# Kernel optimization log

Hardware: AMD Instinct MI355X
Metric: run time of the kernel (lower is better)

The kernel has to match this reference:

```python
import jax, jax.numpy as jnp
import numpy as np
from jax import lax

D_TEMPORAL, D_INNER, D_STATE, D_CONV, DT_RANK = 2, 4, 16, 4, 1
EPS = 1e-5


def setup_inputs() -> dict:
    key = jax.random.key(0)
    ks = jax.random.split(key, 14)
    B, L = 16, 32768
    f = lambda k, s, scale=1.0: jax.random.normal(k, s, jnp.float32) * scale
    dt_b = float(np.log(np.expm1(0.01)))  # softplus^-1(0.01), typical dt init
    A_log = jnp.log(jnp.tile(jnp.arange(1, D_STATE + 1, dtype=jnp.float32), (D_INNER, 1)))
    return {
        "hidden_states": f(ks[0], (B, D_TEMPORAL, L)),
        "norm_w": jnp.ones((D_TEMPORAL,), jnp.float32),
        "in_proj_w": f(ks[1], (2 * D_INNER, D_TEMPORAL), 0.5),
        "conv_w": f(ks[2], (D_INNER, D_CONV), 0.3),
        "conv_b": f(ks[3], (D_INNER,), 0.1),
        "x_proj_w": f(ks[4], (DT_RANK + 2 * D_STATE, D_INNER), 0.3),
        "dt_proj_w": f(ks[5], (D_INNER, DT_RANK), 1.0),
        "dt_proj_b": jnp.full((D_INNER,), dt_b, jnp.float32),
        "A_log": A_log,
        "D": jnp.ones((D_INNER,), jnp.float32),
        "conv_w_b": f(ks[6], (D_INNER, D_CONV), 0.3),
        "conv_b_b": f(ks[7], (D_INNER,), 0.1),
        "x_proj_w_b": f(ks[8], (DT_RANK + 2 * D_STATE, D_INNER), 0.3),
        "dt_proj_w_b": f(ks[9], (D_INNER, DT_RANK), 1.0),
        "dt_proj_b_b": jnp.full((D_INNER,), dt_b, jnp.float32),
        "A_b_log": A_log,
        "D_b": jnp.ones((D_INNER,), jnp.float32),
        "out_proj_w": f(ks[10], (D_TEMPORAL, D_INNER), 0.3),
        "norm_f_w": jnp.ones((D_TEMPORAL,), jnp.float32),
    }


def _silu(x):
    return x * jax.nn.sigmoid(x)


def _rmsnorm(x, w):
    return x * lax.rsqrt(jnp.mean(x * x, axis=-1, keepdims=True) + EPS) * w


def _branch(x, z, conv_w, conv_b, x_proj_w, dt_proj_w, dt_proj_b, A_log, D):
    # x, z: (B, d_inner, L). Causal depthwise conv + silu.
    Bb, d, L = x.shape
    xc = lax.conv_general_dilated(
        x, conv_w[:, None, :], (1,), [(D_CONV - 1, 0)],
        feature_group_count=d, dimension_numbers=("NCH", "OIH", "NCH"))
    u = _silu(xc + conv_b[None, :, None]).transpose(0, 2, 1)      # (B, L, d)
    x_dbl = u @ x_proj_w.T                                        # (B, L, rank+2n)
    dt, Bm, Cm = jnp.split(x_dbl, [DT_RANK, DT_RANK + D_STATE], axis=-1)
    dt = jax.nn.softplus(dt @ dt_proj_w.T + dt_proj_b)            # (B, L, d)
    A = -jnp.exp(A_log)                                           # (d, n)
    dA = jnp.exp(dt[..., None] * A)                               # (B, L, d, n)
    dBu = (dt * u)[..., None] * Bm[:, :, None, :]                 # (B, L, d, n)

    def step(h, inp):
        dA_t, dBu_t, C_t = inp
        h = dA_t * h + dBu_t                                      # (B, d, n)
        return h, jnp.einsum("bdn,bn->bd", h, C_t)

    h0 = jnp.zeros((Bb, d, D_STATE), dtype=u.dtype)
    _, ys = lax.scan(step, h0, (jnp.swapaxes(dA, 0, 1), jnp.swapaxes(dBu, 0, 1), jnp.swapaxes(Cm, 0, 1)))
    y = jnp.swapaxes(ys, 0, 1) + u * D                            # (B, L, d)
    return y * _silu(z.transpose(0, 2, 1))


def _forward(hidden_states, norm_w, in_proj_w, conv_w, conv_b, x_proj_w, dt_proj_w,
             dt_proj_b, A_log, D, conv_w_b, conv_b_b, x_proj_w_b, dt_proj_w_b,
             dt_proj_b_b, A_b_log, D_b, out_proj_w, norm_f_w):
    # hidden_states: (B, T=d_temporal, L); scan runs over L.
    hs = jnp.swapaxes(hidden_states, 1, 2)                        # (B, L, T)
    residual = hs.astype(jnp.float32)
    hs = _rmsnorm(residual, norm_w)
    xz = jnp.swapaxes(hs @ in_proj_w.T, 1, 2)                     # (B, 2*d_inner, L)
    x, z = jnp.split(xz, 2, axis=1)
    y_f = _branch(x, z, conv_w, conv_b, x_proj_w, dt_proj_w, dt_proj_b, A_log, D)
    y_b = _branch(x[..., ::-1], z[..., ::-1], conv_w_b, conv_b_b, x_proj_w_b,
                  dt_proj_w_b, dt_proj_b_b, A_b_log, D_b)
    y = y_f + y_b[:, ::-1, :]                                     # (B, L, d_inner)
    out = y @ out_proj_w.T                                        # (B, L, T)
    out = _rmsnorm(out + residual, norm_f_w)
    return jnp.swapaxes(out, 1, 2)                                # (B, T, L)


def reference(hidden_states, norm_w, in_proj_w, conv_w, conv_b, x_proj_w, dt_proj_w,
              dt_proj_b, A_log, D, conv_w_b, conv_b_b, x_proj_w_b, dt_proj_w_b,
              dt_proj_b_b, A_b_log, D_b, out_proj_w, norm_f_w):
    return _forward(hidden_states, norm_w, in_proj_w, conv_w, conv_b, x_proj_w,
                    dt_proj_w, dt_proj_b, A_log, D, conv_w_b, conv_b_b, x_proj_w_b,
                    dt_proj_w_b, dt_proj_b_b, A_b_log, D_b, out_proj_w, norm_f_w)
```

## Files before the change

kernel.cpp:

```cpp
#include <hip/hip_runtime.h>
#include <hip/hip_bf16.h>
#include <cstdint>

#define BB 16
#define LL 32768
#define NC 512

#define WD_SZ 256
#define XPW 0
#define CVW 132
#define CVB 148
#define DTW 152
#define DTB 156
#define AW  160
#define DW  224
#define G_INPROJ 512
#define G_NORMW 528
#define G_OUTP 530
#define G_NORMF 538
#define FLG 1000

#define PQ_OFF 4096
#define PQ_BYTES ((size_t)BB*2*NC*64*8)
#define HIN_OFF (PQ_OFF + PQ_BYTES)

__device__ __forceinline__ float bf2f(unsigned short u){ return __uint_as_float(((unsigned int)u)<<16); }
__device__ __forceinline__ float blo(unsigned int u){ return __uint_as_float(u<<16); }
__device__ __forceinline__ float bhi(unsigned int u){ return __uint_as_float(u & 0xffff0000u); }
__device__ __forceinline__ unsigned short f2bf(float f){
  unsigned int x = __float_as_uint(f);
  x += 0x7fffu + ((x>>16)&1u);
  return (unsigned short)(x>>16);
}
__device__ __forceinline__ unsigned int pack2(float a, float b){
  __hip_bfloat162 h = __float22bfloat162_rn(make_float2(a,b));
  union { __hip_bfloat162 h2; unsigned int u; } cv; cv.h2 = h;
  return cv.u;
}
__device__ __forceinline__ float siluf(float x){
  return x * __builtin_amdgcn_rcpf(1.f + __expf(-x));
}
__device__ __forceinline__ float softplusf_(float x){
  return fmaxf(x,0.f) + 0.69314718056f*__log2f(1.f + __expf(-fabsf(x)));
}
__device__ __forceinline__ float rowsum16(float x){
  union { float f; int i; } a, t;
  a.f = x;
  t.i = __builtin_amdgcn_update_dpp(0, a.i, 0x121, 0xf, 0xf, true); a.f += t.f;
  t.i = __builtin_amdgcn_update_dpp(0, a.i, 0x122, 0xf, 0xf, true); a.f += t.f;
  t.i = __builtin_amdgcn_update_dpp(0, a.i, 0x124, 0xf, 0xf, true); a.f += t.f;
  t.i = __builtin_amdgcn_update_dpp(0, a.i, 0x128, 0xf, 0xf, true); a.f += t.f;
  return a.f;
}
__device__ __forceinline__ float ldw(const void* p, int i, int isf){
  return isf ? ((const float*)p)[i] : bf2f(((const unsigned short*)p)[i]);
}
__device__ __forceinline__ float2 hid2(const void* hid, int isf, int b, int t){
  if (isf){
    const float* p = (const float*)hid;
    return make_float2(p[(size_t)b*2*LL + t], p[(size_t)b*2*LL + LL + t]);
  }
  const unsigned short* p = (const unsigned short*)hid;
  return make_float2(bf2f(p[(size_t)b*2*LL + t]), bf2f(p[(size_t)b*2*LL + LL + t]));
}
__device__ __forceinline__ float4 xrow(const void* __restrict__ hid, int isf,
                                       const float* __restrict__ W, int b, int t){
  float2 h = hid2(hid, isf, b, t);
  float ms = rsqrtf(0.5f*(h.x*h.x + h.y*h.y) + 1e-5f);
  float v0 = h.x*ms*W[G_NORMW], v1 = h.y*ms*W[G_NORMW+1];
  float4 x;
  x.x = W[G_INPROJ+0]*v0 + W[G_INPROJ+1]*v1;
  x.y = W[G_INPROJ+2]*v0 + W[G_INPROJ+3]*v1;
  x.z = W[G_INPROJ+4]*v0 + W[G_INPROJ+5]*v1;
  x.w = W[G_INPROJ+6]*v0 + W[G_INPROJ+7]*v1;
  return x;
}

__global__ void k_prep(const void* __restrict__ normw, const void* __restrict__ inpj,
    const void* __restrict__ cwf, const void* __restrict__ cbf,
    const void* __restrict__ xpf, const void* __restrict__ dwf,
    const void* __restrict__ dbf, const void* __restrict__ alf,
    const void* __restrict__ ddf,
    const void* __restrict__ cwb, const void* __restrict__ cbb,
    const void* __restrict__ xpb, const void* __restrict__ dwb,
    const void* __restrict__ dbb, const void* __restrict__ alb,
    const void* __restrict__ ddb,
    const void* __restrict__ outp, const void* __restrict__ nfw,
    float* __restrict__ W)
{
  const int isf = (((const unsigned int*)ddf)[0] == 0x3F800000u) ? 1 : 0;
  int t = threadIdx.x;
  for (int i=t;i<132;i+=256){ W[XPW+i]=ldw(xpf,i,isf); W[WD_SZ+XPW+i]=ldw(xpb,i,isf); }
  for (int i=t;i<16;i+=256){ W[CVW+i]=ldw(cwf,i,isf); W[WD_SZ+CVW+i]=ldw(cwb,i,isf); W[G_INPROJ+i]=ldw(inpj,i,isf); }
  for (int i=t;i<4;i+=256){
    W[CVB+i]=ldw(cbf,i,isf); W[WD_SZ+CVB+i]=ldw(cbb,i,isf);
    W[DTW+i]=ldw(dwf,i,isf); W[WD_SZ+DTW+i]=ldw(dwb,i,isf);
    W[DTB+i]=ldw(dbf,i,isf); W[WD_SZ+DTB+i]=ldw(dbb,i,isf);
    W[DW+i] =ldw(ddf,i,isf); W[WD_SZ+DW+i] =ldw(ddb,i,isf);
  }
  for (int i=t;i<64;i+=256){
    W[AW+i]       = -__expf(ldw(alf,i,isf)) * 1.44269504089f;
    W[WD_SZ+AW+i] = -__expf(ldw(alb,i,isf)) * 1.44269504089f;
  }
  for (int i=t;i<8;i+=256) W[G_OUTP+i]=ldw(outp,i,isf);
  for (int i=t;i<2;i+=256){ W[G_NORMW+i]=ldw(normw,i,isf); W[G_NORMF+i]=ldw(nfw,i,isf); }
  if (t==0) W[FLG] = (float)isf;
}

__global__ __launch_bounds__(128) void k_chunk(const void* __restrict__ hid,
    const float* __restrict__ W, float2* __restrict__ PQ)
{
  __shared__ __align__(16) unsigned int   DUc[2][2][4*68];
  __shared__ __align__(16) unsigned short Bsc[2][2][16*72];
  __shared__ __align__(16) float4 xbc[2][70];
  const int lane = threadIdx.x & 63;
  const int w    = threadIdx.x >> 6;
  const int gid  = blockIdx.x*2 + w;
  const int c    = gid & (NC-1);
  const int b    = gid >> 9;
  const int isf  = (int)W[FLG];

  {
    int t = c*64 + lane;
    xbc[w][lane+3] = xrow(hid, isf, W, b, t);
    if (lane < 3){
      int t2 = c*64 - 3 + lane;
      float4 v = make_float4(0.f,0.f,0.f,0.f);
      if (t2 >= 0) v = xrow(hid, isf, W, b, t2);
      xbc[w][lane] = v;
    }
    if (lane >= 61){
      int t3 = c*64 + lane + 3;
      float4 v = make_float4(0.f,0.f,0.f,0.f);
      if (t3 < LL) v = xrow(hid, isf, W, b, t3);
      xbc[w][lane+6] = v;
    }
  }
  __syncthreads();
  {
    float4 xk0=xbc[w][lane],xk1=xbc[w][lane+1],xk2=xbc[w][lane+2],xk3=xbc[w][lane+3];
    float4 xk4=xbc[w][lane+4],xk5=xbc[w][lane+5],xk6=xbc[w][lane+6];
    float uf[4], ub[4];
    uf[0] = siluf(W[CVB+0] + W[CVW+ 0]*xk0.x + W[CVW+ 1]*xk1.x + W[CVW+ 2]*xk2.x + W[CVW+ 3]*xk3.x);
    uf[1] = siluf(W[CVB+1] + W[CVW+ 4]*xk0.y + W[CVW+ 5]*xk1.y + W[CVW+ 6]*xk2.y + W[CVW+ 7]*xk3.y);
    uf[2] = siluf(W[CVB+2] + W[CVW+ 8]*xk0.z + W[CVW+ 9]*xk1.z + W[CVW+10]*xk2.z + W[CVW+11]*xk3.z);
    uf[3] = siluf(W[CVB+3] + W[CVW+12]*xk0.w + W[CVW+13]*xk1.w + W[CVW+14]*xk2.w + W[CVW+15]*xk3.w);
    const float* Wb = W + WD_SZ;
    ub[0] = siluf(Wb[CVB+0] + Wb[CVW+ 0]*xk6.x + Wb[CVW+ 1]*xk5.x + Wb[CVW+ 2]*xk4.x + Wb[CVW+ 3]*xk3.x);
    ub[1] = siluf(Wb[CVB+1] + Wb[CVW+ 4]*xk6.y + Wb[CVW+ 5]*xk5.y + Wb[CVW+ 6]*xk4.y + Wb[CVW+ 7]*xk3.y);
    ub[2] = siluf(Wb[CVB+2] + Wb[CVW+ 8]*xk6.z + Wb[CVW+ 9]*xk5.z + Wb[CVW+10]*xk4.z + Wb[CVW+11]*xk3.z);
    ub[3] = siluf(Wb[CVB+3] + Wb[CVW+12]*xk6.w + Wb[CVW+13]*xk5.w + Wb[CVW+14]*xk4.w + Wb[CVW+15]*xk3.w);
    #pragma unroll
    for (int dr=0; dr<2; dr++){
      const float* Wd = W + dr*WD_SZ;
      const float* uu = dr ? ub : uf;
      float dtr = Wd[XPW+0]*uu[0]+Wd[XPW+1]*uu[1]+Wd[XPW+2]*uu[2]+Wd[XPW+3]*uu[3];
      #pragma unroll
      for (int d2=0; d2<4; d2++){
        float dt = softplusf_(fmaf(Wd[DTW+d2], dtr, Wd[DTB+d2]));
        DUc[w][dr][d2*68+lane] = pack2(dt, dt*uu[d2]);
      }
      #pragma unroll
      for (int n=0;n<16;n++){
        float Bn = Wd[XPW+(1+n)*4+0]*uu[0]+Wd[XPW+(1+n)*4+1]*uu[1]
                 + Wd[XPW+(1+n)*4+2]*uu[2]+Wd[XPW+(1+n)*4+3]*uu[3];
        Bsc[w][dr][n*72+lane] = f2bf(Bn);
      }
    }
  }
  __syncthreads();
  const int d = lane>>4, n = lane&15;
  const float Af = W[AW + d*16 + n];
  const float Ab = W[WD_SZ + AW + d*16 + n];
  float Pf=1.f, Qf=0.f, Pb=1.f, Qb=0.f;
  for (int j4=0; j4<16; j4++){
    const int t0f = j4*4, t0b = 60 - j4*4;
    uint4 uf4 = *(const uint4*)&DUc[w][0][d*68+t0f];
    uint4 ub4 = *(const uint4*)&DUc[w][1][d*68+t0b];
    ushort4 bf4 = *(const ushort4*)&Bsc[w][0][n*72+t0f];
    ushort4 bb4 = *(const ushort4*)&Bsc[w][1][n*72+t0b];
    unsigned int ufa[4]={uf4.x,uf4.y,uf4.z,uf4.w}, uba[4]={ub4.x,ub4.y,ub4.z,ub4.w};
    unsigned short bfa[4]={bf4.x,bf4.y,bf4.z,bf4.w}, bba[4]={bb4.x,bb4.y,bb4.z,bb4.w};
    #pragma unroll
    for (int jr=0; jr<4; jr++){
      float e = exp2f(Af*blo(ufa[jr]));
      Pf *= e;
      Qf = fmaf(Qf, e, bhi(ufa[jr])*bf2f(bfa[jr]));
      const int k = 3-jr;
      float eb = exp2f(Ab*blo(uba[k]));
      Pb *= eb;
      Qb = fmaf(Qb, eb, bhi(uba[k])*bf2f(bba[k]));
    }
  }
  PQ[((size_t)(b*2+0)*NC + c)*64 + lane]        = make_float2(Pf,Qf);
  PQ[((size_t)(b*2+1)*NC + (NC-1-c))*64 + lane] = make_float2(Pb,Qb);
}

__global__ __launch_bounds__(512) void k_scan(const float2* __restrict__ PQ, float* __restrict__ hin)
{
  __shared__ float2 seg[8][64];
  const int bd = blockIdx.x;
  const int lane = threadIdx.x & 63;
  const int w = threadIdx.x >> 6;
  const size_t base = (size_t)bd*NC;
  const int c0 = w*64;
  float h = 0.f, R = 1.f;
  for (int cc=0; cc<64; cc+=16){
    float2 v[16];
    #pragma unroll
    for (int k=0;k<16;k++) v[k] = PQ[(base+c0+cc+k)*64+lane];
    #pragma unroll
    for (int k=0;k<16;k++){
      hin[(base+c0+cc+k)*64+lane] = h;
      h = fmaf(v[k].x, h, v[k].y);
      R *= v[k].x;
    }
  }
  seg[w][lane] = make_float2(R, h);
  __syncthreads();
  if (w > 0){
    float init = 0.f;
    #pragma unroll
    for (int s=0; s<7; s++){
      if (s < w){ float2 pq = seg[s][lane]; init = fmaf(pq.x, init, pq.y); }
    }
    float Rr = 1.f;
    for (int cc=0; cc<64; cc+=16){
      float pv[16], hv[16];
      #pragma unroll
      for (int k=0;k<16;k++) pv[k] = PQ[(base+c0+cc+k)*64+lane].x;
      #pragma unroll
      for (int k=0;k<16;k++) hv[k] = hin[(base+c0+cc+k)*64+lane];
      #pragma unroll
      for (int k=0;k<16;k++){
        hin[(base+c0+cc+k)*64+lane] = hv[k] + init*Rr;
        Rr *= pv[k];
      }
    }
  }
}

__global__ __launch_bounds__(128) void k_fused(const void* __restrict__ hid,
    const float* __restrict__ W, const float* __restrict__ hin,
    void* __restrict__ out)
{
  __shared__ __align__(16) unsigned int DUf[2][2][4*68];
  __shared__ __align__(16) unsigned int BCf[2][2][16*68];
  __shared__ __align__(16) float4 xbf[2][70];
  __shared__ __align__(16) float zsf[2][256];
  __shared__ __align__(16) float uDf[2][256];
  __shared__ __align__(16) float ySm[2][256];
  const int lane = threadIdx.x & 63;
  const int w    = threadIdx.x >> 6;
  const int gid  = blockIdx.x*2 + w;
  const int c    = gid & (NC-1);
  const int b    = gid >> 9;
  const int isf  = (int)W[FLG];

  float hF = hin[((size_t)(b*2+0)*NC + c)*64 + lane];
  float hB = hin[((size_t)(b*2+1)*NC + (NC-1-c))*64 + lane];

  {
    int t = c*64 + lane;
    float2 h = hid2(hid, isf, b, t);
    float ms = rsqrtf(0.5f*(h.x*h.x + h.y*h.y) + 1e-5f);
    float v0 = h.x*ms*W[G_NORMW], v1 = h.y*ms*W[G_NORMW+1];
    float4 x;
    x.x = W[G_INPROJ+0]*v0 + W[G_INPROJ+1]*v1;
    x.y = W[G_INPROJ+2]*v0 + W[G_INPROJ+3]*v1;
    x.z = W[G_INPROJ+4]*v0 + W[G_INPROJ+5]*v1;
    x.w = W[G_INPROJ+6]*v0 + W[G_INPROJ+7]*v1;
    xbf[w][lane+3] = x;
    float4 z4;
    z4.x = siluf(W[G_INPROJ+ 8]*v0 + W[G_INPROJ+ 9]*v1);
    z4.y = siluf(W[G_INPROJ+10]*v0 + W[G_INPROJ+11]*v1);
    z4.z = siluf(W[G_INPROJ+12]*v0 + W[G_INPROJ+13]*v1);
    z4.w = siluf(W[G_INPROJ+14]*v0 + W[G_INPROJ+15]*v1);
    *(float4*)&zsf[w][lane*4] = z4;
    if (lane < 3){
      int t2 = c*64 - 3 + lane;
      float4 v = make_float4(0.f,0.f,0.f,0.f);
      if (t2 >= 0) v = xrow(hid, isf, W, b, t2);
      xbf[w][lane] = v;
    }
    if (lane >= 61){
      int t3 = c*64 + lane + 3;
      float4 v = make_float4(0.f,0.f,0.f,0.f);
      if (t3 < LL) v = xrow(hid, isf, W, b, t3);
      xbf[w][lane+6] = v;
    }
  }
  __syncthreads();
  {
    float4 xk0=xbf[w][lane],xk1=xbf[w][lane+1],xk2=xbf[w][lane+2],xk3=xbf[w][lane+3];
    float4 xk4=xbf[w][lane+4],xk5=xbf[w][lane+5],xk6=xbf[w][lane+6];
    float uf[4], ub[4];
    uf[0] = siluf(W[CVB+0] + W[CVW+ 0]*xk0.x + W[CVW+ 1]*xk1.x + W[CVW+ 2]*xk2.x + W[CVW+ 3]*xk3.x);
    uf[1] = siluf(W[CVB+1] + W[CVW+ 4]*xk0.y + W[CVW+ 5]*xk1.y + W[CVW+ 6]*xk2.y + W[CVW+ 7]*xk3.y);
    uf[2] = siluf(W[CVB+2] + W[CVW+ 8]*xk0.z + W[CVW+ 9]*xk1.z + W[CVW+10]*xk2.z + W[CVW+11]*xk3.z);
    uf[3] = siluf(W[CVB+3] + W[CVW+12]*xk0.w + W[CVW+13]*xk1.w + W[CVW+14]*xk2.w + W[CVW+15]*xk3.w);
    const float* Wb = W + WD_SZ;
    ub[0] = siluf(Wb[CVB+0] + Wb[CVW+ 0]*xk6.x + Wb[CVW+ 1]*xk5.x + Wb[CVW+ 2]*xk4.x + Wb[CVW+ 3]*xk3.x);
    ub[1] = siluf(Wb[CVB+1] + Wb[CVW+ 4]*xk6.y + Wb[CVW+ 5]*xk5.y + Wb[CVW+ 6]*xk4.y + Wb[CVW+ 7]*xk3.y);
    ub[2] = siluf(Wb[CVB+2] + Wb[CVW+ 8]*xk6.z + Wb[CVW+ 9]*xk5.z + Wb[CVW+10]*xk4.z + Wb[CVW+11]*xk3.z);
    ub[3] = siluf(Wb[CVB+3] + Wb[CVW+12]*xk6.w + Wb[CVW+13]*xk5.w + Wb[CVW+14]*xk4.w + Wb[CVW+15]*xk3.w);
    *(float4*)&uDf[w][lane*4] = make_float4(
        uf[0]*W[DW+0]+ub[0]*Wb[DW+0], uf[1]*W[DW+1]+ub[1]*Wb[DW+1],
        uf[2]*W[DW+2]+ub[2]*Wb[DW+2], uf[3]*W[DW+3]+ub[3]*Wb[DW+3]);
    #pragma unroll
    for (int dr=0; dr<2; dr++){
      const float* Wd = W + dr*WD_SZ;
      const float* uu = dr ? ub : uf;
      float dtr = Wd[XPW+0]*uu[0]+Wd[XPW+1]*uu[1]+Wd[XPW+2]*uu[2]+Wd[XPW+3]*uu[3];
      #pragma unroll
      for (int d2=0; d2<4; d2++){
        float dt = softplusf_(fmaf(Wd[DTW+d2], dtr, Wd[DTB+d2]));
        DUf[w][dr][d2*68+lane] = pack2(dt, dt*uu[d2]);
      }
      #pragma unroll
      for (int n=0;n<16;n++){
        float Bn = Wd[XPW+(1+n)*4+0]*uu[0]+Wd[XPW+(1+n)*4+1]*uu[1]
                 + Wd[XPW+(1+n)*4+2]*uu[2]+Wd[XPW+(1+n)*4+3]*uu[3];
        float Cn = Wd[XPW+(17+n)*4+0]*uu[0]+Wd[XPW+(17+n)*4+1]*uu[1]
                 + Wd[XPW+(17+n)*4+2]*uu[2]+Wd[XPW+(17+n)*4+3]*uu[3];
        BCf[w][dr][n*68+lane] = pack2(Bn,Cn);
      }
    }
  }
  __syncthreads();

  const int d = lane>>4, n = lane&15;
  {
    const float Af = W[AW + d*16 + n];
    for (int j4=0; j4<16; j4++){
      const int t0 = j4*4;
      uint4 u4 = *(const uint4*)&DUf[w][0][d*68+t0];
      uint4 c4 = *(const uint4*)&BCf[w][0][n*68+t0];
      unsigned int ua[4]={u4.x,u4.y,u4.z,u4.w};
      unsigned int ca[4]={c4.x,c4.y,c4.z,c4.w};
      float s[4];
      #pragma unroll
      for (int jr=0; jr<4; jr++){
        float e = exp2f(Af*blo(ua[jr]));
        hF = fmaf(e, hF, bhi(ua[jr])*blo(ca[jr]));
        s[jr] = rowsum16(hF*bhi(ca[jr]));
      }
      if (n == 0) *(float4*)&ySm[w][d*64+t0] = make_float4(s[0],s[1],s[2],s[3]);
    }
  }
  {
    const float Ab = W[WD_SZ + AW + d*16 + n];
    for (int j4=0; j4<16; j4++){
      const int t0 = 60 - j4*4;
      uint4 u4 = *(const uint4*)&DUf[w][1][d*68+t0];
      uint4 c4 = *(const uint4*)&BCf[w][1][n*68+t0];
      unsigned int ua[4]={u4.x,u4.y,u4.z,u4.w};
      unsigned int ca[4]={c4.x,c4.y,c4.z,c4.w};
      float s[4];
      #pragma unroll
      for (int jr=0; jr<4; jr++){
        const int k = 3-jr;
        float e = exp2f(Ab*blo(ua[k]));
        hB = fmaf(e, hB, bhi(ua[k])*blo(ca[k]));
        s[k] = rowsum16(hB*bhi(ca[k]));
      }
      if (n == 0){
        float4 f = *(const float4*)&ySm[w][d*64+t0];
        *(float4*)&ySm[w][d*64+t0] = make_float4(f.x+s[0],f.y+s[1],f.z+s[2],f.w+s[3]);
      }
    }
  }
  __syncthreads();
  {
    int t = c*64 + lane;
    float4 zz = *(const float4*)&zsf[w][lane*4];
    float4 ud = *(const float4*)&uDf[w][lane*4];
    float y0 = (ySm[w][0*64+lane] + ud.x) * zz.x;
    float y1 = (ySm[w][1*64+lane] + ud.y) * zz.y;
    float y2 = (ySm[w][2*64+lane] + ud.z) * zz.z;
    float y3 = (ySm[w][3*64+lane] + ud.w) * zz.w;
    float o0 = W[G_OUTP+0]*y0 + W[G_OUTP+1]*y1 + W[G_OUTP+2]*y2 + W[G_OUTP+3]*y3;
    float o1 = W[G_OUTP+4]*y0 + W[G_OUTP+5]*y1 + W[G_OUTP+6]*y2 + W[G_OUTP+7]*y3;
    float2 r = hid2(hid, isf, b, t);
    o0 += r.x;
    o1 += r.y;
    float ms = rsqrtf(0.5f*(o0*o0 + o1*o1) + 1e-5f);
    float e0 = o0*ms*W[G_NORMF], e1 = o1*ms*W[G_NORMF+1];
    size_t i0 = (size_t)b*2*LL + t, i1 = i0 + LL;
    if (isf){
      ((float*)out)[i0] = e0;
      ((float*)out)[i1] = e1;
    } else {
      ((unsigned short*)out)[i0] = f2bf(e0);
      ((unsigned short*)out)[i1] = f2bf(e1);
    }
  }
}

extern "C" void kernel_launch(void* const* d_in, const int* in_sizes, int n_in,
                              void* d_out, int out_size, void* d_ws, size_t ws_size,
                              hipStream_t stream)
{
  (void)in_sizes; (void)n_in; (void)out_size; (void)ws_size;
  const void* hid = d_in[0];
  float* W   = (float*)d_ws;
  float2* PQ = (float2*)((char*)d_ws + PQ_OFF);
  float* hin = (float*)((char*)d_ws + HIN_OFF);

  k_prep<<<1,256,0,stream>>>(d_in[1], d_in[2], d_in[3], d_in[4], d_in[5], d_in[6],
                             d_in[7], d_in[8], d_in[9], d_in[10], d_in[11], d_in[12],
                             d_in[13], d_in[14], d_in[15], d_in[16], d_in[17], d_in[18], W);
  k_chunk<<<BB*NC/2, 128, 0, stream>>>(hid, W, PQ);
  k_scan<<<BB*2, 512, 0, stream>>>(PQ, hin);
  k_fused<<<BB*NC/2, 128, 0, stream>>>(hid, W, hin, d_out);
}
```

Measured before the change: 213.2 us.

## Split directions across wavefronts and replace chunk scan with three-phase segmented scan

Each block now handles one chunk, with wavefront 0 running the forward direction and wavefront 1 the backward direction, instead of each wave serially doing both directions for its own chunk. This halves the serial recurrence length per wave and doubles the grid size. The single 32-block inter-chunk scan is replaced by three kernels (segment reduce, segment prefix, segment apply), giving 256-block phases instead of the old second pass that re-read PQ and rewrote hin. The cost is more kernel launches, redundant per-block x computation, and a shared-memory combine of the two directions in the epilogue.

```diff
diff --git a/kernel.cpp b/kernel.cpp
--- a/kernel.cpp
+++ b/kernel.cpp
@@ -23,6 +23,10 @@
 #define PQ_OFF 4096
 #define PQ_BYTES ((size_t)BB*2*NC*64*8)
 #define HIN_OFF (PQ_OFF + PQ_BYTES)
+#define HIN_BYTES ((size_t)BB*2*NC*64*4)
+#define SEG_OFF (HIN_OFF + HIN_BYTES)
+#define SEG_BYTES ((size_t)BB*2*8*64*8)
+#define SEGI_OFF (SEG_OFF + SEG_BYTES)
 
 __device__ __forceinline__ float bf2f(unsigned short u){ return __uint_as_float(((unsigned int)u)<<16); }
 __device__ __forceinline__ float blo(unsigned int u){ return __uint_as_float(u<<16); }
@@ -76,6 +80,22 @@
   return x;
 }
 
+__device__ __forceinline__ void convu(const float4* xb, int lane, const float* Wd, int dr, float* u){
+  if (dr == 0){
+    float4 xk0=xb[lane],xk1=xb[lane+1],xk2=xb[lane+2],xk3=xb[lane+3];
+    u[0] = siluf(Wd[CVB+0] + Wd[CVW+ 0]*xk0.x + Wd[CVW+ 1]*xk1.x + Wd[CVW+ 2]*xk2.x + Wd[CVW+ 3]*xk3.x);
+    u[1] = siluf(Wd[CVB+1] + Wd[CVW+ 4]*xk0.y + Wd[CVW+ 5]*xk1.y + Wd[CVW+ 6]*xk2.y + Wd[CVW+ 7]*xk3.y);
+    u[2] = siluf(Wd[CVB+2] + Wd[CVW+ 8]*xk0.z + Wd[CVW+ 9]*xk1.z + Wd[CVW+10]*xk2.z + Wd[CVW+11]*xk3.z);
+    u[3] = siluf(Wd[CVB+3] + Wd[CVW+12]*xk0.w + Wd[CVW+13]*xk1.w + Wd[CVW+14]*xk2.w + Wd[CVW+15]*xk3.w);
+  } else {
+    float4 xk3=xb[lane+3],xk4=xb[lane+4],xk5=xb[lane+5],xk6=xb[lane+6];
+    u[0] = siluf(Wd[CVB+0] + Wd[CVW+ 0]*xk6.x + Wd[CVW+ 1]*xk5.x + Wd[CVW+ 2]*xk4.x + Wd[CVW+ 3]*xk3.x);
+    u[1] = siluf(Wd[CVB+1] + Wd[CVW+ 4]*xk6.y + Wd[CVW+ 5]*xk5.y + Wd[CVW+ 6]*xk4.y + Wd[CVW+ 7]*xk3.y);
+    u[2] = siluf(Wd[CVB+2] + Wd[CVW+ 8]*xk6.z + Wd[CVW+ 9]*xk5.z + Wd[CVW+10]*xk4.z + Wd[CVW+11]*xk3.z);
+    u[3] = siluf(Wd[CVB+3] + Wd[CVW+12]*xk6.w + Wd[CVW+13]*xk5.w + Wd[CVW+14]*xk4.w + Wd[CVW+15]*xk3.w);
+  }
+}
+
 __global__ void k_prep(const void* __restrict__ normw, const void* __restrict__ inpj,
     const void* __restrict__ cwf, const void* __restrict__ cbf,
     const void* __restrict__ xpf, const void* __restrict__ dwf,
@@ -110,132 +130,117 @@
 __global__ __launch_bounds__(128) void k_chunk(const void* __restrict__ hid,
     const float* __restrict__ W, float2* __restrict__ PQ)
 {
-  __shared__ __align__(16) unsigned int   DUc[2][2][4*68];
-  __shared__ __align__(16) unsigned short Bsc[2][2][16*72];
-  __shared__ __align__(16) float4 xbc[2][70];
+  __shared__ __align__(16) float4 xb[70];
+  __shared__ __align__(16) unsigned int   DU[2][4*68];
+  __shared__ __align__(16) unsigned short Bs[2][16*72];
   const int lane = threadIdx.x & 63;
   const int w    = threadIdx.x >> 6;
-  const int gid  = blockIdx.x*2 + w;
+  const int gid  = blockIdx.x;
   const int c    = gid & (NC-1);
   const int b    = gid >> 9;
   const int isf  = (int)W[FLG];
 
-  {
-    int t = c*64 + lane;
-    xbc[w][lane+3] = xrow(hid, isf, W, b, t);
+  if (w == 0){
+    xb[lane+3] = xrow(hid, isf, W, b, c*64 + lane);
+  } else {
     if (lane < 3){
       int t2 = c*64 - 3 + lane;
       float4 v = make_float4(0.f,0.f,0.f,0.f);
       if (t2 >= 0) v = xrow(hid, isf, W, b, t2);
-      xbc[w][lane] = v;
+      xb[lane] = v;
     }
     if (lane >= 61){
       int t3 = c*64 + lane + 3;
       float4 v = make_float4(0.f,0.f,0.f,0.f);
       if (t3 < LL) v = xrow(hid, isf, W, b, t3);
-      xbc[w][lane+6] = v;
+      xb[lane+6] = v;
     }
   }
   __syncthreads();
+  const float* Wd = W + w*WD_SZ;
   {
-    float4 xk0=xbc[w][lane],xk1=xbc[w][lane+1],xk2=xbc[w][lane+2],xk3=xbc[w][lane+3];
-    float4 xk4=xbc[w][lane+4],xk5=xbc[w][lane+5],xk6=xbc[w][lane+6];
-    float uf[4], ub[4];
-    uf[0] = siluf(W[CVB+0] + W[CVW+ 0]*xk0.x + W[CVW+ 1]*xk1.x + W[CVW+ 2]*xk2.x + W[CVW+ 3]*xk3.x);
-    uf[1] = siluf(W[CVB+1] + W[CVW+ 4]*xk0.y + W[CVW+ 5]*xk1.y + W[CVW+ 6]*xk2.y + W[CVW+ 7]*xk3.y);
-    uf[2] = siluf(W[CVB+2] + W[CVW+ 8]*xk0.z + W[CVW+ 9]*xk1.z + W[CVW+10]*xk2.z + W[CVW+11]*xk3.z);
-    uf[3] = siluf(W[CVB+3] + W[CVW+12]*xk0.w + W[CVW+13]*xk1.w + W[CVW+14]*xk2.w + W[CVW+15]*xk3.w);
-    const float* Wb = W + WD_SZ;
-    ub[0] = siluf(Wb[CVB+0] + Wb[CVW+ 0]*xk6.x + Wb[CVW+ 1]*xk5.x + Wb[CVW+ 2]*xk4.x + Wb[CVW+ 3]*xk3.x);
-    ub[1] = siluf(Wb[CVB+1] + Wb[CVW+ 4]*xk6.y + Wb[CVW+ 5]*xk5.y + Wb[CVW+ 6]*xk4.y + Wb[CVW+ 7]*xk3.y);
-    ub[2] = siluf(Wb[CVB+2] + Wb[CVW+ 8]*xk6.z + Wb[CVW+ 9]*xk5.z + Wb[CVW+10]*xk4.z + Wb[CVW+11]*xk3.z);
-    ub[3] = siluf(Wb[CVB+3] + Wb[CVW+12]*xk6.w + Wb[CVW+13]*xk5.w + Wb[CVW+14]*xk4.w + Wb[CVW+15]*xk3.w);
-    #pragma unroll
-    for (int dr=0; dr<2; dr++){
-      const float* Wd = W + dr*WD_SZ;
-      const float* uu = dr ? ub : uf;
-      float dtr = Wd[XPW+0]*uu[0]+Wd[XPW+1]*uu[1]+Wd[XPW+2]*uu[2]+Wd[XPW+3]*uu[3];
-      #pragma unroll
-      for (int d2=0; d2<4; d2++){
-        float dt = softplusf_(fmaf(Wd[DTW+d2], dtr, Wd[DTB+d2]));
-        DUc[w][dr][d2*68+lane] = pack2(dt, dt*uu[d2]);
-      }
-      #pragma unroll
-      for (int n=0;n<16;n++){
-        float Bn = Wd[XPW+(1+n)*4+0]*uu[0]+Wd[XPW+(1+n)*4+1]*uu[1]
-                 + Wd[XPW+(1+n)*4+2]*uu[2]+Wd[XPW+(1+n)*4+3]*uu[3];
-        Bsc[w][dr][n*72+lane] = f2bf(Bn);
-      }
-    }
-  }
-  __syncthreads();
+    float u[4];
+    convu(xb, lane, Wd, w, u);
+    float dtr = Wd[XPW+0]*u[0]+Wd[XPW+1]*u[1]+Wd[XPW+2]*u[2]+Wd[XPW+3]*u[3];
+    #pragma unroll
+    for (int d2=0; d2<4; d2++){
+      float dt = softplusf_(fmaf(Wd[DTW+d2], dtr, Wd[DTB+d2]));
+      DU[w][d2*68+lane] = pack2(dt, dt*u[d2]);
+    }
+    #pragma unroll
+    for (int n=0;n<16;n++){
+      float Bn = Wd[XPW+(1+n)*4+0]*u[0]+Wd[XPW+(1+n)*4+1]*u[1]
+               + Wd[XPW+(1+n)*4+2]*u[2]+Wd[XPW+(1+n)*4+3]*u[3];
+      Bs[w][n*72+lane] = f2bf(Bn);
+    }
+  }
   const int d = lane>>4, n = lane&15;
-  const float Af = W[AW + d*16 + n];
-  const float Ab = W[WD_SZ + AW + d*16 + n];
-  float Pf=1.f, Qf=0.f, Pb=1.f, Qb=0.f;
+  const float A2 = Wd[AW + d*16 + n];
+  float P=1.f, Q=0.f;
   for (int j4=0; j4<16; j4++){
-    const int t0f = j4*4, t0b = 60 - j4*4;
-    uint4 uf4 = *(const uint4*)&DUc[w][0][d*68+t0f];
-    uint4 ub4 = *(const uint4*)&DUc[w][1][d*68+t0b];
-    ushort4 bf4 = *(const ushort4*)&Bsc[w][0][n*72+t0f];
-    ushort4 bb4 = *(const ushort4*)&Bsc[w][1][n*72+t0b];
-    unsigned int ufa[4]={uf4.x,uf4.y,uf4.z,uf4.w}, uba[4]={ub4.x,ub4.y,ub4.z,ub4.w};
-    unsigned short bfa[4]={bf4.x,bf4.y,bf4.z,bf4.w}, bba[4]={bb4.x,bb4.y,bb4.z,bb4.w};
+    const int t0 = w ? (60 - j4*4) : (j4*4);
+    uint4 u4 = *(const uint4*)&DU[w][d*68+t0];
+    ushort4 b4 = *(const ushort4*)&Bs[w][n*72+t0];
+    unsigned int ua[4]={u4.x,u4.y,u4.z,u4.w};
+    unsigned short ba[4]={b4.x,b4.y,b4.z,b4.w};
     #pragma unroll
     for (int jr=0; jr<4; jr++){
-      float e = exp2f(Af*blo(ufa[jr]));
-      Pf *= e;
-      Qf = fmaf(Qf, e, bhi(ufa[jr])*bf2f(bfa[jr]));
-      const int k = 3-jr;
-      float eb = exp2f(Ab*blo(uba[k]));
-      Pb *= eb;
-      Qb = fmaf(Qb, eb, bhi(uba[k])*bf2f(bba[k]));
-    }
-  }
-  PQ[((size_t)(b*2+0)*NC + c)*64 + lane]        = make_float2(Pf,Qf);
-  PQ[((size_t)(b*2+1)*NC + (NC-1-c))*64 + lane] = make_float2(Pb,Qb);
-}
-
-__global__ __launch_bounds__(512) void k_scan(const float2* __restrict__ PQ, float* __restrict__ hin)
-{
-  __shared__ float2 seg[8][64];
-  const int bd = blockIdx.x;
-  const int lane = threadIdx.x & 63;
-  const int w = threadIdx.x >> 6;
-  const size_t base = (size_t)bd*NC;
-  const int c0 = w*64;
-  float h = 0.f, R = 1.f;
+      const int k = w ? (3-jr) : jr;
+      float e = exp2f(A2*blo(ua[k]));
+      P *= e;
+      Q = fmaf(Q, e, bhi(ua[k])*bf2f(ba[k]));
+    }
+  }
+  const int cs = w ? (NC-1-c) : c;
+  PQ[((size_t)(b*2+w)*NC + cs)*64 + lane] = make_float2(P,Q);
+}
+
+__global__ __launch_bounds__(64) void k_scan1(const float2* __restrict__ PQ, float2* __restrict__ SEG)
+{
+  const int blk = blockIdx.x;
+  const int bd = blk>>3, s = blk&7;
+  const int lane = threadIdx.x;
+  const size_t base = (size_t)bd*NC + s*64;
+  float R=1.f, H=0.f;
   for (int cc=0; cc<64; cc+=16){
     float2 v[16];
     #pragma unroll
-    for (int k=0;k<16;k++) v[k] = PQ[(base+c0+cc+k)*64+lane];
+    for (int k=0;k<16;k++) v[k] = PQ[(base+cc+k)*64+lane];
+    #pragma unroll
+    for (int k=0;k<16;k++){ H = fmaf(v[k].x, H, v[k].y); R *= v[k].x; }
+  }
+  SEG[(size_t)blk*64+lane] = make_float2(R,H);
+}
+
+__global__ __launch_bounds__(64) void k_scan2(const float2* __restrict__ SEG, float* __restrict__ SEGI)
+{
+  const int bd = blockIdx.x;
+  const int lane = threadIdx.x;
+  float h = 0.f;
+  #pragma unroll
+  for (int s=0;s<8;s++){
+    SEGI[((size_t)bd*8+s)*64+lane] = h;
+    float2 rh = SEG[((size_t)bd*8+s)*64+lane];
+    h = fmaf(rh.x, h, rh.y);
+  }
+}
+
+__global__ __launch_bounds__(64) void k_scan3(const float2* __restrict__ PQ,
+    const float* __restrict__ SEGI, float* __restrict__ hin)
+{
+  const int blk = blockIdx.x;
+  const int bd = blk>>3, s = blk&7;
+  const int lane = threadIdx.x;
+  const size_t base = (size_t)bd*NC + s*64;
+  float h = SEGI[(size_t)blk*64+lane];
+  for (int cc=0; cc<64; cc+=16){
+    float2 v[16];
+    #pragma unroll
+    for (int k=0;k<16;k++) v[k] = PQ[(base+cc+k)*64+lane];
     #pragma unroll
     for (int k=0;k<16;k++){
-      hin[(base+c0+cc+k)*64+lane] = h;
+      hin[(base+cc+k)*64+lane] = h;
       h = fmaf(v[k].x, h, v[k].y);
-      R *= v[k].x;
-    }
-  }
-  seg[w][lane] = make_float2(R, h);
-  __syncthreads();
-  if (w > 0){
-    float init = 0.f;
-    #pragma unroll
-    for (int s=0; s<7; s++){
-      if (s < w){ float2 pq = seg[s][lane]; init = fmaf(pq.x, init, pq.y); }
-    }
-    float Rr = 1.f;
-    for (int cc=0; cc<64; cc+=16){
-      float pv[16], hv[16];
-      #pragma unroll
-      for (int k=0;k<16;k++) pv[k] = PQ[(base+c0+cc+k)*64+lane].x;
-      #pragma unroll
-      for (int k=0;k<16;k++) hv[k] = hin[(base+c0+cc+k)*64+lane];
-      #pragma unroll
-      for (int k=0;k<16;k++){
-        hin[(base+c0+cc+k)*64+lane] = hv[k] + init*Rr;
-        Rr *= pv[k];
-      }
     }
   }
 }
@@ -244,23 +249,23 @@
     const float* __restrict__ W, const float* __restrict__ hin,
     void* __restrict__ out)
 {
-  __shared__ __align__(16) unsigned int DUf[2][2][4*68];
-  __shared__ __align__(16) unsigned int BCf[2][2][16*68];
-  __shared__ __align__(16) float4 xbf[2][70];
-  __shared__ __align__(16) float zsf[2][256];
-  __shared__ __align__(16) float uDf[2][256];
-  __shared__ __align__(16) float ySm[2][256];
+  __shared__ __align__(16) float4 xb[70];
+  __shared__ __align__(16) unsigned int DU[2][4*68];
+  __shared__ __align__(16) unsigned int BC[2][16*68];
+  __shared__ __align__(16) float zs[256];
+  __shared__ __align__(16) float uD[2][256];
+  __shared__ __align__(16) float yS[2][4*68];
   const int lane = threadIdx.x & 63;
   const int w    = threadIdx.x >> 6;
-  const int gid  = blockIdx.x*2 + w;
+  const int gid  = blockIdx.x;
   const int c    = gid & (NC-1);
   const int b    = gid >> 9;
   const int isf  = (int)W[FLG];
 
-  float hF = hin[((size_t)(b*2+0)*NC + c)*64 + lane];
-  float hB = hin[((size_t)(b*2+1)*NC + (NC-1-c))*64 + lane];
-
-  {
+  const int cs = w ? (NC-1-c) : c;
+  float hS = hin[((size_t)(b*2+w)*NC + cs)*64 + lane];
+
+  if (w == 0){
     int t = c*64 + lane;
     float2 h = hid2(hid, isf, b, t);
     float ms = rsqrtf(0.5f*(h.x*h.x + h.y*h.y) + 1e-5f);
@@ -270,115 +275,78 @@
     x.y = W[G_INPROJ+2]*v0 + W[G_INPROJ+3]*v1;
     x.z = W[G_INPROJ+4]*v0 + W[G_INPROJ+5]*v1;
     x.w = W[G_INPROJ+6]*v0 + W[G_INPROJ+7]*v1;
-    xbf[w][lane+3] = x;
+    xb[lane+3] = x;
     float4 z4;
     z4.x = siluf(W[G_INPROJ+ 8]*v0 + W[G_INPROJ+ 9]*v1);
     z4.y = siluf(W[G_INPROJ+10]*v0 + W[G_INPROJ+11]*v1);
     z4.z = siluf(W[G_INPROJ+12]*v0 + W[G_INPROJ+13]*v1);
     z4.w = siluf(W[G_INPROJ+14]*v0 + W[G_INPROJ+15]*v1);
-    *(float4*)&zsf[w][lane*4] = z4;
+    *(float4*)&zs[lane*4] = z4;
+  } else {
     if (lane < 3){
       int t2 = c*64 - 3 + lane;
       float4 v = make_float4(0.f,0.f,0.f,0.f);
       if (t2 >= 0) v = xrow(hid, isf, W, b, t2);
-      xbf[w][lane] = v;
+      xb[lane] = v;
     }
     if (lane >= 61){
       int t3 = c*64 + lane + 3;
       float4 v = make_float4(0.f,0.f,0.f,0.f);
       if (t3 < LL) v = xrow(hid, isf, W, b, t3);
-      xbf[w][lane+6] = v;
+      xb[lane+6] = v;
     }
   }
   __syncthreads();
+  const float* Wd = W + w*WD_SZ;
   {
-    float4 xk0=xbf[w][lane],xk1=xbf[w][lane+1],xk2=xbf[w][lane+2],xk3=xbf[w][lane+3];
-    float4 xk4=xbf[w][lane+4],xk5=xbf[w][lane+5],xk6=xbf[w][lane+6];
-    float uf[4], ub[4];
-    uf[0] = siluf(W[CVB+0] + W[CVW+ 0]*xk0.x + W[CVW+ 1]*xk1.x + W[CVW+ 2]*xk2.x + W[CVW+ 3]*xk3.x);
-    uf[1] = siluf(W[CVB+1] + W[CVW+ 4]*xk0.y + W[CVW+ 5]*xk1.y + W[CVW+ 6]*xk2.y + W[CVW+ 7]*xk3.y);
-    uf[2] = siluf(W[CVB+2] + W[CVW+ 8]*xk0.z + W[CVW+ 9]*xk1.z + W[CVW+10]*xk2.z + W[CVW+11]*xk3.z);
-    uf[3] = siluf(W[CVB+3] + W[CVW+12]*xk0.w + W[CVW+13]*xk1.w + W[CVW+14]*xk2.w + W[CVW+15]*xk3.w);
-    const float* Wb = W + WD_SZ;
-    ub[0] = siluf(Wb[CVB+0] + Wb[CVW+ 0]*xk6.x + Wb[CVW+ 1]*xk5.x + Wb[CVW+ 2]*xk4.x + Wb[CVW+ 3]*xk3.x);
-    ub[1] = siluf(Wb[CVB+1] + Wb[CVW+ 4]*xk6.y + Wb[CVW+ 5]*xk5.y + Wb[CVW+ 6]*xk4.y + Wb[CVW+ 7]*xk3.y);
-    ub[2] = siluf(Wb[CVB+2] + Wb[CVW+ 8]*xk6.z + Wb[CVW+ 9]*xk5.z + Wb[CVW+10]*xk4.z + Wb[CVW+11]*xk3.z);
-    ub[3] = siluf(Wb[CVB+3] + Wb[CVW+12]*xk6.w + Wb[CVW+13]*xk5.w + Wb[CVW+14]*xk4.w + Wb[CVW+15]*xk3.w);
-    *(float4*)&uDf[w][lane*4] = make_float4(
-        uf[0]*W[DW+0]+ub[0]*Wb[DW+0], uf[1]*W[DW+1]+ub[1]*Wb[DW+1],
-        uf[2]*W[DW+2]+ub[2]*Wb[DW+2], uf[3]*W[DW+3]+ub[3]*Wb[DW+3]);
-    #pragma unroll
-    for (int dr=0; dr<2; dr++){
-      const float* Wd = W + dr*WD_SZ;
-      const float* uu = dr ? ub : uf;
-      float dtr = Wd[XPW+0]*uu[0]+Wd[XPW+1]*uu[1]+Wd[XPW+2]*uu[2]+Wd[XPW+3]*uu[3];
-      #pragma unroll
-      for (int d2=0; d2<4; d2++){
-        float dt = softplusf_(fmaf(Wd[DTW+d2], dtr, Wd[DTB+d2]));
-        DUf[w][dr][d2*68+lane] = pack2(dt, dt*uu[d2]);
-      }
-      #pragma unroll
-      for (int n=0;n<16;n++){
-        float Bn = Wd[XPW+(1+n)*4+0]*uu[0]+Wd[XPW+(1+n)*4+1]*uu[1]
-                 + Wd[XPW+(1+n)*4+2]*uu[2]+Wd[XPW+(1+n)*4+3]*uu[3];
-        float Cn = Wd[XPW+(17+n)*4+0]*uu[0]+Wd[XPW+(17+n)*4+1]*uu[1]
-                 + Wd[XPW+(17+n)*4+2]*uu[2]+Wd[XPW+(17+n)*4+3]*uu[3];
-        BCf[w][dr][n*68+lane] = pack2(Bn,Cn);
-      }
-    }
-  }
-  __syncthreads();
-
-  const int d = lane>>4, n = lane&15;
+    float u[4];
+    convu(xb, lane, Wd, w, u);
+    *(float4*)&uD[w][lane*4] = make_float4(u[0]*Wd[DW+0], u[1]*Wd[DW+1], u[2]*Wd[DW+2], u[3]*Wd[DW+3]);
+    float dtr = Wd[XPW+0]*u[0]+Wd[XPW+1]*u[1]+Wd[XPW+2]*u[2]+Wd[XPW+3]*u[3];
+    #pragma unroll
+    for (int d2=0; d2<4; d2++){
+      float dt = softplusf_(fmaf(Wd[DTW+d2], dtr, Wd[DTB+d2]));
+      DU[w][d2*68+lane] = pack2(dt, dt*u[d2]);
+    }
+    #pragma unroll
+    for (int n=0;n<16;n++){
+      float Bn = Wd[XPW+(1+n)*4+0]*u[0]+Wd[XPW+(1+n)*4+1]*u[1]
+               + Wd[XPW+(1+n)*4+2]*u[2]+Wd[XPW+(1+n)*4+3]*u[3];
+      float Cn = Wd[XPW+(17+n)*4+0]*u[0]+Wd[XPW+(17+n)*4+1]*u[1]
+               + Wd[XPW+(17+n)*4+2]*u[2]+Wd[XPW+(17+n)*4+3]*u[3];
+      BC[w][n*68+lane] = pack2(Bn,Cn);
+    }
+  }
   {
-    const float Af = W[AW + d*16 + n];
+    const int d = lane>>4, n = lane&15;
+    const float A2 = Wd[AW + d*16 + n];
     for (int j4=0; j4<16; j4++){
-      const int t0 = j4*4;
-      uint4 u4 = *(const uint4*)&DUf[w][0][d*68+t0];
-      uint4 c4 = *(const uint4*)&BCf[w][0][n*68+t0];
+      const int t0 = w ? (60 - j4*4) : (j4*4);
+      uint4 u4 = *(const uint4*)&DU[w][d*68+t0];
+      uint4 c4 = *(const uint4*)&BC[w][n*68+t0];
       unsigned int ua[4]={u4.x,u4.y,u4.z,u4.w};
       unsigned int ca[4]={c4.x,c4.y,c4.z,c4.w};
       float s[4];
       #pragma unroll
       for (int jr=0; jr<4; jr++){
-        float e = exp2f(Af*blo(ua[jr]));
-        hF = fmaf(e, hF, bhi(ua[jr])*blo(ca[jr]));
-        s[jr] = rowsum16(hF*bhi(ca[jr]));
+        const int k = w ? (3-jr) : jr;
+        float e = exp2f(A2*blo(ua[k]));
+        hS = fmaf(e, hS, bhi(ua[k])*blo(ca[k]));
+        s[k] = rowsum16(hS*bhi(ca[k]));
       }
-      if (n == 0) *(float4*)&ySm[w][d*64+t0] = make_float4(s[0],s[1],s[2],s[3]);
-    }
-  }
-  {
-    const float Ab = W[WD_SZ + AW + d*16 + n];
-    for (int j4=0; j4<16; j4++){
-      const int t0 = 60 - j4*4;
-      uint4 u4 = *(const uint4*)&DUf[w][1][d*68+t0];
-      uint4 c4 = *(const uint4*)&BCf[w][1][n*68+t0];
-      unsigned int ua[4]={u4.x,u4.y,u4.z,u4.w};
-      unsigned int ca[4]={c4.x,c4.y,c4.z,c4.w};
-      float s[4];
-      #pragma unroll
-      for (int jr=0; jr<4; jr++){
-        const int k = 3-jr;
-        float e = exp2f(Ab*blo(ua[k]));
-        hB = fmaf(e, hB, bhi(ua[k])*blo(ca[k]));
-        s[k] = rowsum16(hB*bhi(ca[k]));
-      }
-      if (n == 0){
-        float4 f = *(const float4*)&ySm[w][d*64+t0];
-        *(float4*)&ySm[w][d*64+t0] = make_float4(f.x+s[0],f.y+s[1],f.z+s[2],f.w+s[3]);
-      }
+      if (n == 0) *(float4*)&yS[w][d*68+t0] = make_float4(s[0],s[1],s[2],s[3]);
     }
   }
   __syncthreads();
-  {
+  if (w == 0){
     int t = c*64 + lane;
-    float4 zz = *(const float4*)&zsf[w][lane*4];
-    float4 ud = *(const float4*)&uDf[w][lane*4];
-    float y0 = (ySm[w][0*64+lane] + ud.x) * zz.x;
-    float y1 = (ySm[w][1*64+lane] + ud.y) * zz.y;
-    float y2 = (ySm[w][2*64+lane] + ud.z) * zz.z;
-    float y3 = (ySm[w][3*64+lane] + ud.w) * zz.w;
+    float4 zz = *(const float4*)&zs[lane*4];
+    float4 u0 = *(const float4*)&uD[0][lane*4];
+    float4 u1 = *(const float4*)&uD[1][lane*4];
+    float y0 = (yS[0][0*68+lane] + yS[1][0*68+lane] + u0.x + u1.x) * zz.x;
+    float y1 = (yS[0][1*68+lane] + yS[1][1*68+lane] + u0.y + u1.y) * zz.y;
+    float y2 = (yS[0][2*68+lane] + yS[1][2*68+lane] + u0.z + u1.z) * zz.z;
+    float y3 = (yS[0][3*68+lane] + yS[1][3*68+lane] + u0.w + u1.w) * zz.w;
     float o0 = W[G_OUTP+0]*y0 + W[G_OUTP+1]*y1 + W[G_OUTP+2]*y2 + W[G_OUTP+3]*y3;
     float o1 = W[G_OUTP+4]*y0 + W[G_OUTP+5]*y1 + W[G_OUTP+6]*y2 + W[G_OUTP+7]*y3;
     float2 r = hid2(hid, isf, b, t);
@@ -403,14 +371,18 @@
 {
   (void)in_sizes; (void)n_in; (void)out_size; (void)ws_size;
   const void* hid = d_in[0];
-  float* W   = (float*)d_ws;
-  float2* PQ = (float2*)((char*)d_ws + PQ_OFF);
-  float* hin = (float*)((char*)d_ws + HIN_OFF);
+  float* W     = (float*)d_ws;
+  float2* PQ   = (float2*)((char*)d_ws + PQ_OFF);
+  float* hin   = (float*)((char*)d_ws + HIN_OFF);
+  float2* SEG  = (float2*)((char*)d_ws + SEG_OFF);
+  float* SEGI  = (float*)((char*)d_ws + SEGI_OFF);
 
   k_prep<<<1,256,0,stream>>>(d_in[1], d_in[2], d_in[3], d_in[4], d_in[5], d_in[6],
                              d_in[7], d_in[8], d_in[9], d_in[10], d_in[11], d_in[12],
                              d_in[13], d_in[14], d_in[15], d_in[16], d_in[17], d_in[18], W);
-  k_chunk<<<BB*NC/2, 128, 0, stream>>>(hid, W, PQ);
-  k_scan<<<BB*2, 512, 0, stream>>>(PQ, hin);
-  k_fused<<<BB*NC/2, 128, 0, stream>>>(hid, W, hin, d_out);
-}
+  k_chunk<<<BB*NC, 128, 0, stream>>>(hid, W, PQ);
+  k_scan1<<<BB*2*8, 64, 0, stream>>>(PQ, SEG);
+  k_scan2<<<BB*2, 64, 0, stream>>>(SEG, SEGI);
+  k_scan3<<<BB*2*8, 64, 0, stream>>>(PQ, SEGI, hin);
+  k_fused<<<BB*NC, 128, 0, stream>>>(hid, W, hin, d_out);
+}
```

New measurement: 217.0 us. No clear change (+1.8%).
